# Kernel tuning notes

Hardware: AMD Instinct MI355X
Metric: run time of the kernel (lower is better)

## Reference

```python
import jax, jax.numpy as jnp
import numpy as np

PATCH = 5
PAD = PATCH // 2
EPS = 0.01
NP2 = PATCH * PATCH  # 25 elements per patch


def _conv(x, w, b):
    # VALID conv, NCHW / OIHW
    y = jax.lax.conv_general_dilated(x, w, (1, 1), 'VALID',
                                     dimension_numbers=('NCHW', 'OIHW', 'NCHW'))
    return y + b[None, :, None, None]


def _maxpool2(x):
    return jax.lax.reduce_window(x, -jnp.inf, jax.lax.max,
                                 (1, 1, 2, 2), (1, 1, 2, 2), 'VALID')


def _normed_patches(x):
    # x: [B,C,H,W] -> zero-mean unit-std 5x5 patches [B,C,H,W,25]
    B, C, H, W = x.shape
    xp = jnp.pad(x, ((0, 0), (0, 0), (PAD, PAD), (PAD, PAD)))
    p = jnp.stack([xp[:, :, u:u + H, v:v + W]
                   for u in range(PATCH) for v in range(PATCH)], axis=-1)
    mu = p.mean(axis=-1, keepdims=True)
    sd = p.std(axis=-1, keepdims=True)
    return (p - mu) / (sd + EPS)


def _normxcorr(X, Y):
    # patch-wise NCC: each 5x5 patch of X at (i,j) vs patches of Y at rows
    # i-2..i+2 (zero outside) and ALL W columns -> [B, C*5*W, H, W]
    B, C, H, W = X.shape
    Xn = _normed_patches(X)            # [B,C,H,W,25]
    Yn = _normed_patches(Y)            # [B,C,H,W,25]
    Ynp = jnp.pad(Yn, ((0, 0), (0, 0), (PAD, PAD), (0, 0), (0, 0)))
    # row-shifted views: d=0..4 corresponds to displacement d-2
    Ysh = jnp.stack([Ynp[:, :, d:d + H] for d in range(PATCH)], axis=2)  # [B,C,5,H,W,25]
    out = jnp.einsum('bcijp,bcdikp->bcdkij', Xn, Ysh) / NP2  # [B,C,5,W,H,W]
    return out.reshape(B, C * PATCH * W, H, W)  # C*5*12 = 1500 channels


def _branch(x, w1, b1, w2, b2):
    x = _maxpool2(jax.nn.relu(_conv(x, w1, b1)))
    x = _maxpool2(jax.nn.relu(_conv(x, w2, b2)))
    return x  # [B,25,37,12]


def setup_inputs() -> dict:
    key = jax.random.key(0)
    ks = jax.random.split(key, 10)
    B = 64

    def n(k, shp, s=0.05):
        return jax.random.normal(k, shp, dtype=jnp.float32) * s

    return {
        'x1': jax.random.normal(ks[0], (B, 3, 160, 60), dtype=jnp.float32),
        'x2': jax.random.normal(ks[1], (B, 3, 160, 60), dtype=jnp.float32),
        'w_conv1': n(ks[2], (20, 3, 5, 5)), 'b_conv1': jnp.zeros((20,), jnp.float32),
        'w_conv2': n(ks[3], (25, 20, 5, 5)), 'b_conv2': jnp.zeros((25,), jnp.float32),
        'w_red1': n(ks[4], (25, 1500, 1, 1)), 'b_red1': jnp.zeros((25,), jnp.float32),
        'w_red2': n(ks[5], (25, 25, 3, 3)), 'b_red2': jnp.zeros((25,), jnp.float32),
        'w_lin1': n(ks[6], (500, 25 * 17 * 5)), 'b_lin1': jnp.zeros((500,), jnp.float32),
        'w_lin2': n(ks[7], (2, 500)), 'b_lin2': jnp.zeros((2,), jnp.float32),
    }


def reference(x1, x2, w_conv1, b_conv1, w_conv2, b_conv2,
              w_red1, b_red1, w_red2, b_red2,
              w_lin1, b_lin1, w_lin2, b_lin2):
    f1 = _branch(x1, w_conv1, b_conv1, w_conv2, b_conv2)  # [B,25,37,12]
    f2 = _branch(x2, w_conv1, b_conv1, w_conv2, b_conv2)
    r = jax.nn.relu(_normxcorr(f1, f2))                   # [B,1500,37,12]
    r = jax.nn.relu(_conv(r, w_red1, b_red1))             # [B,25,37,12]
    r = _maxpool2(_conv(r, w_red2, b_red2))               # [B,25,17,5]
    r = r.reshape(r.shape[0], -1)                         # [B,2125]
    r = r @ w_lin1.T + b_lin1
    r = r @ w_lin2.T + b_lin2
    return r
```

## Files before the change

### kernel.cpp

```cpp
#include <hip/hip_runtime.h>
#include <math.h>


static const long OFF_C1   = 0;
static const long OFF_F    = 5591040;
static const long OFF_MU   = 7011840;
static const long OFF_IV   = 8432640;
static const long OFF_WLT  = 9853440;
static const long OFF_PART = 0;
static const long OFF_RED1 = 3552000;
static const long OFF_R2P  = 4262400;
static const long OFF_WR1T = 4500000;
static const long OFF_LINP = 0;

__global__ void k_wt(const float* __restrict__ wl1, float* __restrict__ wlt) {
  long idx = (long)blockIdx.x * 256 + threadIdx.x;
  if (idx < 2125L * 500) {
    long t = idx / 500, o = idx % 500;
    wlt[idx] = wl1[o * 2125 + t];
  }
}

__global__ void k_wrt(const float* __restrict__ wr1, float* __restrict__ wr1t) {
  int idx = blockIdx.x * 256 + threadIdx.x;
  if (idx < 37500) {
    int o = idx / 1500, t = idx % 1500;
    wr1t[t * 25 + o] = wr1[idx];
  }
}

__global__ __launch_bounds__(128) void k_conv1(
    const float* __restrict__ x1, const float* __restrict__ x2,
    const float* __restrict__ w, const float* __restrict__ bias,
    float* __restrict__ out) {
  int img = blockIdx.x;
  int g   = blockIdx.y;
  int oc0 = blockIdx.z * 5;
  int p0  = g * 13;
  const float* x = (img < 64) ? (x1 + (long)img * 28800)
                              : (x2 + (long)(img - 64) * 28800);
  for (int item = threadIdx.x; item < 13 * 28; item += 128) {
    int r = item / 28, j = item % 28;
    int ci0 = 2 * (p0 + r), cj0 = 2 * j;
    float acc[5][4];
#pragma unroll
    for (int o = 0; o < 5; ++o) {
      acc[o][0] = 0.f; acc[o][1] = 0.f; acc[o][2] = 0.f; acc[o][3] = 0.f;
    }
    for (int ic = 0; ic < 3; ++ic) {
      const float* xp = x + (long)ic * 9600 + ci0 * 60 + cj0;
      float win[6][6];
#pragma unroll
      for (int u = 0; u < 6; ++u)
#pragma unroll
        for (int v = 0; v < 6; ++v) win[u][v] = xp[u * 60 + v];
#pragma unroll
      for (int o = 0; o < 5; ++o) {
        const float* wq = w + ((oc0 + o) * 3 + ic) * 25;
#pragma unroll
        for (int u = 0; u < 5; ++u)
#pragma unroll
          for (int v = 0; v < 5; ++v) {
            float wv = wq[u * 5 + v];
            acc[o][0] += wv * win[u][v];
            acc[o][1] += wv * win[u][v + 1];
            acc[o][2] += wv * win[u + 1][v];
            acc[o][3] += wv * win[u + 1][v + 1];
          }
      }
    }
#pragma unroll
    for (int o = 0; o < 5; ++o) {
      float mx = fmaxf(fmaxf(acc[o][0], acc[o][1]), fmaxf(acc[o][2], acc[o][3]));
      out[((long)img * 20 + oc0 + o) * 2184 + (p0 + r) * 28 + j] =
          fmaxf(mx + bias[oc0 + o], 0.f);
    }
  }
}

__global__ __launch_bounds__(128) void k_conv2(
    const float* __restrict__ in, const float* __restrict__ w,
    const float* __restrict__ bias, float* __restrict__ out) {
  int img = blockIdx.x;
  int g   = blockIdx.y;
  int oc0 = blockIdx.z * 5;
  int p0  = g * 10;
  int ROWS = min(10, 37 - p0);
  int tid = threadIdx.x;
  int r = tid / 12, j = tid % 12;
  if (tid >= 120 || r >= ROWS) return;
  const float* x = in + (long)img * 20 * 2184;
  int ci0 = 2 * (p0 + r), cj0 = 2 * j;
  float acc[5][4];
#pragma unroll
  for (int o = 0; o < 5; ++o) {
    acc[o][0] = 0.f; acc[o][1] = 0.f; acc[o][2] = 0.f; acc[o][3] = 0.f;
  }
  for (int ic = 0; ic < 20; ++ic) {
    const float* xp = x + (long)ic * 2184 + ci0 * 28 + cj0;
    float win[6][6];
#pragma unroll
    for (int u = 0; u < 6; ++u)
#pragma unroll
      for (int v = 0; v < 6; ++v) win[u][v] = xp[u * 28 + v];
#pragma unroll
    for (int o = 0; o < 5; ++o) {
      const float* wq = w + ((oc0 + o) * 20 + ic) * 25;
#pragma unroll
      for (int u = 0; u < 5; ++u)
#pragma unroll
        for (int v = 0; v < 5; ++v) {
          float wv = wq[u * 5 + v];
          acc[o][0] += wv * win[u][v];
          acc[o][1] += wv * win[u][v + 1];
          acc[o][2] += wv * win[u + 1][v];
          acc[o][3] += wv * win[u + 1][v + 1];
        }
    }
  }
#pragma unroll
  for (int o = 0; o < 5; ++o) {
    float mx = fmaxf(fmaxf(acc[o][0], acc[o][1]), fmaxf(acc[o][2], acc[o][3]));
    out[((long)img * 25 + oc0 + o) * 444 + (p0 + r) * 12 + j] =
        fmaxf(mx + bias[oc0 + o], 0.f);
  }
}

__global__ __launch_bounds__(448) void k_stats(
    const float* __restrict__ f, float* __restrict__ mu, float* __restrict__ iv) {
  int img = blockIdx.x, c = blockIdx.y;
  int t = threadIdx.x;
  if (t >= 444) return;
  int i = t / 12, j = t % 12;
  const float* fp = f + ((long)img * 25 + c) * 444;
  float s = 0.f, sq = 0.f;
#pragma unroll
  for (int u = 0; u < 5; ++u) {
    int gi = i + u - 2;
    if (gi < 0 || gi >= 37) continue;
#pragma unroll
    for (int v = 0; v < 5; ++v) {
      int gj = j + v - 2;
      if (gj < 0 || gj >= 12) continue;
      float vv = fp[gi * 12 + gj];
      s += vv;
      sq += vv * vv;
    }
  }
  float m = s * 0.04f;
  float var = sq * 0.04f - m * m;
  float sd = sqrtf(fmaxf(var, 0.f));
  long idx = ((long)img * 25 + c) * 444 + t;
  mu[idx] = m;
  iv[idx] = 1.f / (sd + 0.01f);
}

__global__ __launch_bounds__(128) void k_ncc(
    const float* __restrict__ f, const float* __restrict__ mu,
    const float* __restrict__ iv, const float* __restrict__ wr1t,
    float* __restrict__ part) {
  int b  = blockIdx.x;
  int g  = blockIdx.y;
  int cz = blockIdx.z;
  int i0 = g * 10;
  int ROWS = min(10, 37 - i0);
  int tid = threadIdx.x;
  int j = tid % 12, r = tid / 12;
  bool active = (r < ROWS);

  __shared__ float Xt[5][14][16], Yt[5][18][16];
  __shared__ float mX[5][10][12], iX[5][10][12];
  __shared__ float mY[5][14][12], iY[5][14][12];

  const float* Xf = f + (long)b * 25 * 444;
  const float* Yf = f + (long)(64 + b) * 25 * 444;
  const float* muX_g = mu + (long)b * 25 * 444;
  const float* ivX_g = iv + (long)b * 25 * 444;
  const float* muY_g = mu + (long)(64 + b) * 25 * 444;
  const float* ivY_g = iv + (long)(64 + b) * 25 * 444;

#pragma unroll 1
  for (int cc = 0; cc < 5; ++cc) {
    int c = cz * 5 + cc;
    for (int idx = tid; idx < 14 * 16; idx += 128) {
      int rr = idx >> 4, cl = idx & 15;
      int gi = i0 - 2 + rr, gj = cl - 2;
      Xt[cc][rr][cl] = (gi >= 0 && gi < 37 && gj >= 0 && gj < 12)
                           ? Xf[c * 444 + gi * 12 + gj] : 0.f;
    }
    for (int idx = tid; idx < 18 * 16; idx += 128) {
      int rr = idx >> 4, cl = idx & 15;
      int gi = i0 - 4 + rr, gj = cl - 2;
      Yt[cc][rr][cl] = (gi >= 0 && gi < 37 && gj >= 0 && gj < 12)
                           ? Yf[c * 444 + gi * 12 + gj] : 0.f;
    }
    for (int idx = tid; idx < 120; idx += 128) {
      int rr = idx / 12, gj = idx % 12;
      int gi = i0 + rr;
      bool ok = gi < 37;
      mX[cc][rr][gj] = ok ? muX_g[c * 444 + gi * 12 + gj] : 0.f;
      iX[cc][rr][gj] = ok ? ivX_g[c * 444 + gi * 12 + gj] : 0.f;
    }
    for (int idx = tid; idx < 168; idx += 128) {
      int rr = idx / 12, gj = idx % 12;
      int gi = i0 - 2 + rr;
      bool ok = (gi >= 0 && gi < 37);
      float muv = ok ? muY_g[c * 444 + gi * 12 + gj] : 0.f;
      float ivv = ok ? ivY_g[c * 444 + gi * 12 + gj] : 0.f;
      mY[cc][rr][gj] = muv * ivv;
      iY[cc][rr][gj] = ivv;
    }
  }
  __syncthreads();

  float acc[25];
#pragma unroll
  for (int o = 0; o < 25; ++o) acc[o] = 0.f;

  if (active) {
#pragma unroll 1
    for (int cc = 0; cc < 5; ++cc) {
      int c = cz * 5 + cc;
      float xp[5][5];
#pragma unroll
      for (int u = 0; u < 5; ++u)
#pragma unroll
        for (int v = 0; v < 5; ++v) xp[u][v] = Xt[cc][r + u][j + v];
      float muXv = mX[cc][r][j], ivXv = iX[cc][r][j];
      float sX = ivXv * 0.04f;
      float tX = muXv * ivXv;
      const float* wb = wr1t + c * 1500;
#pragma unroll 1
      for (int d = 0; d < 5; ++d) {
        int yi = i0 + r + d - 2;
        if (yi < 0 || yi >= 37) continue;
        float win[5][5];
#pragma unroll
        for (int u = 0; u < 5; ++u)
#pragma unroll
          for (int v = 0; v < 5; ++v) win[u][v] = Yt[cc][r + d + u][v];
#pragma unroll
        for (int k = 0; k < 12; ++k) {
          if (k > 0) {
#pragma unroll
            for (int u = 0; u < 5; ++u) {
#pragma unroll
              for (int v = 0; v < 4; ++v) win[u][v] = win[u][v + 1];
              win[u][4] = Yt[cc][r + d + u][k + 4];
            }
          }
          float rd[5];
#pragma unroll
          for (int u = 0; u < 5; ++u) {
            rd[u] = xp[u][0] * win[u][0];
#pragma unroll
            for (int v = 1; v < 5; ++v) rd[u] = fmaf(xp[u][v], win[u][v], rd[u]);
          }
          float dot = ((rd[0] + rd[1]) + (rd[2] + rd[3])) + rd[4];
          float ivYv = iY[cc][r + d][k];
          float miYv = mY[cc][r + d][k];
          float rv = fmaxf(fmaf(-tX, miYv, dot * sX * ivYv), 0.f);
          const float* wo = wb + (d * 12 + k) * 25;
#pragma unroll
          for (int o = 0; o < 25; ++o) acc[o] = fmaf(wo[o], rv, acc[o]);
        }
      }
    }
  }

  if (active) {
    int i = i0 + r;
    float* p = part + ((long)(b * 5 + cz) * 25) * 444 + i * 12 + j;
#pragma unroll
    for (int o = 0; o < 25; ++o) p[o * 444] = acc[o];
  }
}

__global__ __launch_bounds__(256) void k_red1sum(
    const float* __restrict__ part, const float* __restrict__ b1,
    float* __restrict__ red1) {
  int b = blockIdx.x;
  for (int item = threadIdx.x; item < 25 * 444; item += 256) {
    int o = item / 444, px = item % 444;
    float s = b1[o];
#pragma unroll
    for (int cz = 0; cz < 5; ++cz)
      s += part[((long)(b * 5 + cz) * 25 + o) * 444 + px];
    red1[((long)b * 25 + o) * 444 + px] = fmaxf(s, 0.f);
  }
}

__global__ __launch_bounds__(256) void k_red2(
    const float* __restrict__ red1, const float* __restrict__ w,
    const float* __restrict__ bias, float* __restrict__ r2p) {
  int b = blockIdx.x;
  __shared__ float inb[25 * 444];
  __shared__ float wl[25 * 25 * 9];
  for (int idx = threadIdx.x; idx < 25 * 444; idx += 256)
    inb[idx] = red1[(long)b * 25 * 444 + idx];
  for (int idx = threadIdx.x; idx < 25 * 25 * 9; idx += 256)
    wl[idx] = w[idx];
  __syncthreads();
  for (int item = threadIdx.x; item < 25 * 85; item += 256) {
    int oc = item / 85, rem = item % 85;
    int pi = rem / 5, pj = rem % 5;
    int ci0 = 2 * pi, cj0 = 2 * pj;
    float a00 = 0, a01 = 0, a10 = 0, a11 = 0;
    for (int ic = 0; ic < 25; ++ic) {
      const float* xp = inb + ic * 444 + ci0 * 12 + cj0;
      float win[4][4];
#pragma unroll
      for (int u = 0; u < 4; ++u)
#pragma unroll
        for (int v = 0; v < 4; ++v) win[u][v] = xp[u * 12 + v];
      const float* wq = wl + (oc * 25 + ic) * 9;
#pragma unroll
      for (int u = 0; u < 3; ++u)
#pragma unroll
        for (int v = 0; v < 3; ++v) {
          float wv = wq[u * 3 + v];
          a00 += wv * win[u][v];
          a01 += wv * win[u][v + 1];
          a10 += wv * win[u + 1][v];
          a11 += wv * win[u + 1][v + 1];
        }
    }
    float mx = fmaxf(fmaxf(a00, a01), fmaxf(a10, a11));
    r2p[(long)b * 2125 + item] = mx + bias[oc];
  }
}

__global__ __launch_bounds__(256) void k_lin1p(
    const float* __restrict__ r2p, const float* __restrict__ wlt,
    float* __restrict__ part) {
  int nb = blockIdx.x;
  int kc = blockIdx.y;
  int o0 = nb * 64, t0 = kc * 125;
  int tid = threadIdx.x;
  __shared__ float Xs[64][126];
  __shared__ float Ws[125][64];
  for (int idx = tid; idx < 64 * 125; idx += 256) {
    int b = idx / 125, tt = idx % 125;
    Xs[b][tt] = r2p[(long)b * 2125 + t0 + tt];
  }
  for (int idx = tid; idx < 125 * 64; idx += 256) {
    int tt = idx / 64, oo = idx % 64;
    int o = o0 + oo;
    Ws[tt][oo] = (o < 500) ? wlt[(long)(t0 + tt) * 500 + o] : 0.f;
  }
  __syncthreads();
  int b0 = (tid >> 4) << 2;
  int ol = (tid & 15) << 2;
  float acc[4][4];
#pragma unroll
  for (int i = 0; i < 4; ++i)
#pragma unroll
    for (int q = 0; q < 4; ++q) acc[i][q] = 0.f;
  for (int tt = 0; tt < 125; ++tt) {
    float xv[4];
#pragma unroll
    for (int i = 0; i < 4; ++i) xv[i] = Xs[b0 + i][tt];
    float4 wv = *reinterpret_cast<const float4*>(&Ws[tt][ol]);
#pragma unroll
    for (int i = 0; i < 4; ++i) {
      acc[i][0] += xv[i] * wv.x;
      acc[i][1] += xv[i] * wv.y;
      acc[i][2] += xv[i] * wv.z;
      acc[i][3] += xv[i] * wv.w;
    }
  }
#pragma unroll
  for (int i = 0; i < 4; ++i)
#pragma unroll
    for (int q = 0; q < 4; ++q)
      part[((long)kc * 64 + (b0 + i)) * 512 + o0 + ol + q] = acc[i][q];
}

__global__ __launch_bounds__(512) void k_lin2(
    const float* __restrict__ part, const float* __restrict__ bl1,
    const float* __restrict__ wl2, const float* __restrict__ bl2,
    float* __restrict__ out) {
  int b = blockIdx.x;
  int o = threadIdx.x;
  float s = 0.f;
  if (o < 500) {
#pragma unroll
    for (int kc = 0; kc < 17; ++kc) s += part[((long)kc * 64 + b) * 512 + o];
    s += bl1[o];
  }
  __shared__ float red0[512], red1s[512];
  red0[o]  = (o < 500) ? s * wl2[o] : 0.f;
  red1s[o] = (o < 500) ? s * wl2[500 + o] : 0.f;
  __syncthreads();
  for (int st = 256; st >= 1; st >>= 1) {
    if (o < st) { red0[o] += red0[o + st]; red1s[o] += red1s[o + st]; }
    __syncthreads();
  }
  if (o == 0) {
    out[b * 2 + 0] = red0[0] + bl2[0];
    out[b * 2 + 1] = red1s[0] + bl2[1];
  }
}

extern "C" void kernel_launch(void* const* d_in, const int* in_sizes, int n_in,
                              void* d_out, int out_size, void* d_ws, size_t ws_size,
                              hipStream_t stream) {
  const float* x1   = (const float*)d_in[0];
  const float* x2   = (const float*)d_in[1];
  const float* w1   = (const float*)d_in[2];
  const float* b1   = (const float*)d_in[3];
  const float* w2   = (const float*)d_in[4];
  const float* b2   = (const float*)d_in[5];
  const float* wr1  = (const float*)d_in[6];
  const float* br1  = (const float*)d_in[7];
  const float* wr2  = (const float*)d_in[8];
  const float* br2  = (const float*)d_in[9];
  const float* wl1  = (const float*)d_in[10];
  const float* bl1  = (const float*)d_in[11];
  const float* wl2  = (const float*)d_in[12];
  const float* bl2  = (const float*)d_in[13];
  float* out = (float*)d_out;
  float* ws  = (float*)d_ws;

  float* c1    = ws + OFF_C1;
  float* f     = ws + OFF_F;
  float* mu    = ws + OFF_MU;
  float* iv    = ws + OFF_IV;
  float* wlt   = ws + OFF_WLT;
  float* part  = ws + OFF_PART;
  float* red1  = ws + OFF_RED1;
  float* r2p   = ws + OFF_R2P;
  float* wr1t  = ws + OFF_WR1T;
  float* linp  = ws + OFF_LINP;

  hipLaunchKernelGGL(k_wt, dim3((2125 * 500 + 255) / 256), dim3(256), 0, stream, wl1, wlt);

  hipLaunchKernelGGL(k_conv1, dim3(128, 6, 4), dim3(128), 0, stream, x1, x2, w1, b1, c1);
  hipLaunchKernelGGL(k_conv2, dim3(128, 4, 5), dim3(128), 0, stream, c1, w2, b2, f);

  hipLaunchKernelGGL(k_wrt, dim3(147), dim3(256), 0, stream, wr1, wr1t);

  hipLaunchKernelGGL(k_stats, dim3(128, 25), dim3(448), 0, stream, f, mu, iv);
  hipLaunchKernelGGL(k_ncc, dim3(64, 4, 5), dim3(128), 0, stream, f, mu, iv, wr1t, part);
  hipLaunchKernelGGL(k_red1sum, dim3(64), dim3(256), 0, stream, part, br1, red1);
  hipLaunchKernelGGL(k_red2, dim3(64), dim3(256), 0, stream, red1, wr2, br2, r2p);

  hipLaunchKernelGGL(k_lin1p, dim3(8, 17), dim3(256), 0, stream, r2p, wlt, linp);
  hipLaunchKernelGGL(k_lin2, dim3(64), dim3(512), 0, stream, linp, bl1, wl2, bl2, out);
}
```

Measured before the change: 351.9 us.

## Stage conv inputs in double-buffered shared tiles and vectorize NCC weight loads

```diff
diff --git a/kernel.cpp b/kernel.cpp
--- a/kernel.cpp
+++ b/kernel.cpp
@@ -25,7 +25,7 @@
   int idx = blockIdx.x * 256 + threadIdx.x;
   if (idx < 37500) {
     int o = idx / 1500, t = idx % 1500;
-    wr1t[t * 25 + o] = wr1[idx];
+    wr1t[t * 28 + o] = wr1[idx];
   }
 }
 
@@ -37,23 +37,47 @@
   int g   = blockIdx.y;
   int oc0 = blockIdx.z * 5;
   int p0  = g * 13;
+  int R0  = 2 * p0;
+  int tid = threadIdx.x;
   const float* x = (img < 64) ? (x1 + (long)img * 28800)
                               : (x2 + (long)(img - 64) * 28800);
-  for (int item = threadIdx.x; item < 13 * 28; item += 128) {
-    int r = item / 28, j = item % 28;
-    int ci0 = 2 * (p0 + r), cj0 = 2 * j;
-    float acc[5][4];
-#pragma unroll
-    for (int o = 0; o < 5; ++o) {
-      acc[o][0] = 0.f; acc[o][1] = 0.f; acc[o][2] = 0.f; acc[o][3] = 0.f;
-    }
-    for (int ic = 0; ic < 3; ++ic) {
-      const float* xp = x + (long)ic * 9600 + ci0 * 60 + cj0;
+  __shared__ float tile[2][30][60];
+
+  {
+    const float* src = x + R0 * 60;
+    for (int idx = tid; idx < 1800; idx += 128) {
+      int row = idx / 60, col = idx - row * 60;
+      tile[0][row][col] = src[idx];
+    }
+  }
+
+  float acc[3][5][4];
+#pragma unroll
+  for (int it = 0; it < 3; ++it)
+#pragma unroll
+    for (int o = 0; o < 5; ++o)
+#pragma unroll
+      for (int q = 0; q < 4; ++q) acc[it][o][q] = 0.f;
+
+  for (int ic = 0; ic < 3; ++ic) {
+    __syncthreads();
+    if (ic < 2) {
+      const float* src = x + (ic + 1) * 9600 + R0 * 60;
+      float* dst = &tile[(ic + 1) & 1][0][0];
+      for (int idx = tid; idx < 1800; idx += 128) dst[idx] = src[idx];
+    }
+    int cur = ic & 1;
+#pragma unroll 1
+    for (int it = 0; it < 3; ++it) {
+      int item = tid + it * 128;
+      if (item >= 364) break;
+      int r = item / 28, j = item % 28;
+      int lr = 2 * r, lc = 2 * j;
       float win[6][6];
 #pragma unroll
       for (int u = 0; u < 6; ++u)
 #pragma unroll
-        for (int v = 0; v < 6; ++v) win[u][v] = xp[u * 60 + v];
+        for (int v = 0; v < 6; ++v) win[u][v] = tile[cur][lr + u][lc + v];
 #pragma unroll
       for (int o = 0; o < 5; ++o) {
         const float* wq = w + ((oc0 + o) * 3 + ic) * 25;
@@ -62,16 +86,24 @@
 #pragma unroll
           for (int v = 0; v < 5; ++v) {
             float wv = wq[u * 5 + v];
-            acc[o][0] += wv * win[u][v];
-            acc[o][1] += wv * win[u][v + 1];
-            acc[o][2] += wv * win[u + 1][v];
-            acc[o][3] += wv * win[u + 1][v + 1];
+            acc[it][o][0] = fmaf(wv, win[u][v], acc[it][o][0]);
+            acc[it][o][1] = fmaf(wv, win[u][v + 1], acc[it][o][1]);
+            acc[it][o][2] = fmaf(wv, win[u + 1][v], acc[it][o][2]);
+            acc[it][o][3] = fmaf(wv, win[u + 1][v + 1], acc[it][o][3]);
           }
       }
     }
+  }
+
+#pragma unroll
+  for (int it = 0; it < 3; ++it) {
+    int item = tid + it * 128;
+    if (item >= 364) break;
+    int r = item / 28, j = item % 28;
 #pragma unroll
     for (int o = 0; o < 5; ++o) {
-      float mx = fmaxf(fmaxf(acc[o][0], acc[o][1]), fmaxf(acc[o][2], acc[o][3]));
+      float mx = fmaxf(fmaxf(acc[it][o][0], acc[it][o][1]),
+                       fmaxf(acc[it][o][2], acc[it][o][3]));
       out[((long)img * 20 + oc0 + o) * 2184 + (p0 + r) * 28 + j] =
           fmaxf(mx + bias[oc0 + o], 0.f);
     }
@@ -86,43 +118,70 @@
   int oc0 = blockIdx.z * 5;
   int p0  = g * 10;
   int ROWS = min(10, 37 - p0);
+  int R0  = 2 * p0;
+  int NR  = 2 * ROWS + 4;
   int tid = threadIdx.x;
   int r = tid / 12, j = tid % 12;
-  if (tid >= 120 || r >= ROWS) return;
-  const float* x = in + (long)img * 20 * 2184;
-  int ci0 = 2 * (p0 + r), cj0 = 2 * j;
+  bool active = (tid < 120) && (r < ROWS);
+  const float* xin = in + (long)img * 43680;
+  __shared__ float tile[2][24][29];
+
+  {
+    const float* src = xin + R0 * 28;
+    for (int idx = tid; idx < NR * 28; idx += 128) {
+      int row = idx / 28, col = idx - row * 28;
+      tile[0][row][col] = src[idx];
+    }
+  }
+
   float acc[5][4];
 #pragma unroll
   for (int o = 0; o < 5; ++o) {
     acc[o][0] = 0.f; acc[o][1] = 0.f; acc[o][2] = 0.f; acc[o][3] = 0.f;
   }
+  int lr = 2 * r, lc = 2 * j;
+
   for (int ic = 0; ic < 20; ++ic) {
-    const float* xp = x + (long)ic * 2184 + ci0 * 28 + cj0;
-    float win[6][6];
-#pragma unroll
-    for (int u = 0; u < 6; ++u)
-#pragma unroll
-      for (int v = 0; v < 6; ++v) win[u][v] = xp[u * 28 + v];
+    __syncthreads();
+    if (ic < 19) {
+      const float* src = xin + (ic + 1) * 2184 + R0 * 28;
+      int nxt = (ic + 1) & 1;
+      for (int idx = tid; idx < NR * 28; idx += 128) {
+        int row = idx / 28, col = idx - row * 28;
+        tile[nxt][row][col] = src[idx];
+      }
+    }
+    if (active) {
+      int cur = ic & 1;
+      float win[6][6];
+#pragma unroll
+      for (int u = 0; u < 6; ++u)
+#pragma unroll
+        for (int v = 0; v < 6; ++v) win[u][v] = tile[cur][lr + u][lc + v];
+#pragma unroll
+      for (int o = 0; o < 5; ++o) {
+        const float* wq = w + ((oc0 + o) * 20 + ic) * 25;
+#pragma unroll
+        for (int u = 0; u < 5; ++u)
+#pragma unroll
+          for (int v = 0; v < 5; ++v) {
+            float wv = wq[u * 5 + v];
+            acc[o][0] = fmaf(wv, win[u][v], acc[o][0]);
+            acc[o][1] = fmaf(wv, win[u][v + 1], acc[o][1]);
+            acc[o][2] = fmaf(wv, win[u + 1][v], acc[o][2]);
+            acc[o][3] = fmaf(wv, win[u + 1][v + 1], acc[o][3]);
+          }
+      }
+    }
+  }
+
+  if (active) {
 #pragma unroll
     for (int o = 0; o < 5; ++o) {
-      const float* wq = w + ((oc0 + o) * 20 + ic) * 25;
-#pragma unroll
-      for (int u = 0; u < 5; ++u)
-#pragma unroll
-        for (int v = 0; v < 5; ++v) {
-          float wv = wq[u * 5 + v];
-          acc[o][0] += wv * win[u][v];
-          acc[o][1] += wv * win[u][v + 1];
-          acc[o][2] += wv * win[u + 1][v];
-          acc[o][3] += wv * win[u + 1][v + 1];
-        }
-    }
-  }
-#pragma unroll
-  for (int o = 0; o < 5; ++o) {
-    float mx = fmaxf(fmaxf(acc[o][0], acc[o][1]), fmaxf(acc[o][2], acc[o][3]));
-    out[((long)img * 25 + oc0 + o) * 444 + (p0 + r) * 12 + j] =
-        fmaxf(mx + bias[oc0 + o], 0.f);
+      float mx = fmaxf(fmaxf(acc[o][0], acc[o][1]), fmaxf(acc[o][2], acc[o][3]));
+      out[((long)img * 25 + oc0 + o) * 444 + (p0 + r) * 12 + j] =
+          fmaxf(mx + bias[oc0 + o], 0.f);
+    }
   }
 }
 
@@ -168,7 +227,7 @@
   int j = tid % 12, r = tid / 12;
   bool active = (r < ROWS);
 
-  __shared__ float Xt[5][14][16], Yt[5][18][16];
+  __shared__ float Xt[5][14][17], Yt[5][18][17];
   __shared__ float mX[5][10][12], iX[5][10][12];
   __shared__ float mY[5][14][12], iY[5][14][12];
 
@@ -229,7 +288,7 @@
       float muXv = mX[cc][r][j], ivXv = iX[cc][r][j];
       float sX = ivXv * 0.04f;
       float tX = muXv * ivXv;
-      const float* wb = wr1t + c * 1500;
+      const float* wb = wr1t + c * 1680;
 #pragma unroll 1
       for (int d = 0; d < 5; ++d) {
         int yi = i0 + r + d - 2;
@@ -260,9 +319,17 @@
           float ivYv = iY[cc][r + d][k];
           float miYv = mY[cc][r + d][k];
           float rv = fmaxf(fmaf(-tX, miYv, dot * sX * ivYv), 0.f);
-          const float* wo = wb + (d * 12 + k) * 25;
-#pragma unroll
-          for (int o = 0; o < 25; ++o) acc[o] = fmaf(wo[o], rv, acc[o]);
+          const float* wrow = wb + (d * 12 + k) * 28;
+          float wv[25];
+          *reinterpret_cast<float4*>(&wv[0])  = *reinterpret_cast<const float4*>(wrow);
+          *reinterpret_cast<float4*>(&wv[4])  = *reinterpret_cast<const float4*>(wrow + 4);
+          *reinterpret_cast<float4*>(&wv[8])  = *reinterpret_cast<const float4*>(wrow + 8);
+          *reinterpret_cast<float4*>(&wv[12]) = *reinterpret_cast<const float4*>(wrow + 12);
+          *reinterpret_cast<float4*>(&wv[16]) = *reinterpret_cast<const float4*>(wrow + 16);
+          *reinterpret_cast<float4*>(&wv[20]) = *reinterpret_cast<const float4*>(wrow + 20);
+          wv[24] = wrow[24];
+#pragma unroll
+          for (int o = 0; o < 25; ++o) acc[o] = fmaf(wv[o], rv, acc[o]);
         }
       }
     }
```

New measurement: 447.9 us. +27.3%, slower.
